# Kernel tuning notes

Hardware: AMD Instinct MI355X
Metric: run time of the kernel (lower is better)

Reference implementation:

```python
import math
import jax, jax.numpy as jnp
import numpy as np

B, S, IN = 2, 2048, 2048
HID, H = 2048, 16
D = HID // H  # 128, dim_per_head


def setup_inputs() -> dict:
    key = jax.random.key(0)
    k1, k2, k3, k4 = jax.random.split(key, 4)
    x = jax.random.normal(k1, (B, S, IN), dtype=jnp.float32)
    # nn.Linear(input_size, hidden_size, bias=False) weights: [out, in]
    w_scale = 0.02
    Wq = jax.random.normal(k2, (HID, IN), dtype=jnp.float32) * w_scale
    Wk = jax.random.normal(k3, (HID, IN), dtype=jnp.float32) * w_scale
    Wv = jax.random.normal(k4, (HID, IN), dtype=jnp.float32) * w_scale
    return {"x": x, "Wq": Wq, "Wk": Wk, "Wv": Wv}


def reference(x, Wq, Wk, Wv):
    b, s, _ = x.shape
    scale = 1.0 / math.sqrt(D)
    # query projection over all query chunks at once (chunking is a pure reshape)
    q = (x @ Wq.T) * scale              # [b, s, hid]
    q = q.reshape(b, s, H, D)           # flattened query chunks: bqhd
    # key/value projections; the python loop over 64 kv chunks is just a
    # partition of the seq axis, so computing all chunks at once is identical
    k = (x @ Wk.T).reshape(b, s, H, D)  # bkhd
    v = (x @ Wv.T).reshape(b, s, H, D)  # computed then discarded by the module
    # per-chunk einsum 'bqhd,bkhd->bqhk' concatenated over kv chunks == full scores
    attn_weights = jnp.einsum('bqhd,bkhd->bqhk', q, k)  # [b, s, H, s]
    # the original module discards all of the above and returns zeros
    attn_output = jnp.zeros((b, s, HID), dtype=x.dtype)
    return attn_output, attn_weights
```

## Files before the change

kernel.cpp:

```cpp
#include <hip/hip_runtime.h>
#include <hip/hip_bf16.h>
#include <cstdint>
#include <cmath>

typedef __bf16 bf16_t;
typedef __attribute__((ext_vector_type(8))) bf16_t bf16x8;
typedef __attribute__((ext_vector_type(4))) float f32x4;

#define AS_GLOBAL(p) ((const __attribute__((address_space(1))) void*)(p))
#define AS_LDS(p)    ((__attribute__((address_space(3))) void*)(p))

__device__ __forceinline__ unsigned short f2bf(float f) {
  unsigned u = __builtin_bit_cast(unsigned, f);
  u += 0x7FFFu + ((u >> 16) & 1u);
  return (unsigned short)(u >> 16);
}

#define N4_X  2097152
#define N4_W  1048576
#define N4_Z  2097152
__global__ void cvt3z_kernel(const float* __restrict__ x, const float* __restrict__ wq,
                             const float* __restrict__ wk, ushort4* __restrict__ xb4,
                             ushort4* __restrict__ wb4, float4* __restrict__ zero4,
                             float scale) {
  int i = blockIdx.x * blockDim.x + threadIdx.x;
  int stride = gridDim.x * blockDim.x;
  const int total = N4_X + 2 * N4_W + N4_Z;
  for (; i < total; i += stride) {
    if (i < N4_X + 2 * N4_W) {
      const float4* src;
      ushort4* dst;
      float sc = 1.0f;
      if (i < N4_X) {
        src = reinterpret_cast<const float4*>(x) + i;
        dst = xb4 + i;
      } else if (i < N4_X + N4_W) {
        src = reinterpret_cast<const float4*>(wq) + (i - N4_X);
        dst = wb4 + (i - N4_X);
        sc = scale;
      } else {
        src = reinterpret_cast<const float4*>(wk) + (i - N4_X - N4_W);
        dst = wb4 + (i - N4_X);
      }
      float4 v = *src;
      ushort4 o;
      o.x = f2bf(v.x * sc);
      o.y = f2bf(v.y * sc);
      o.z = f2bf(v.z * sc);
      o.w = f2bf(v.w * sc);
      *dst = o;
    } else {
      zero4[i - (N4_X + 2 * N4_W)] = float4{0.f, 0.f, 0.f, 0.f};
    }
  }
}

#define PM 4096
#define PN 4096
#define PK 2048
#define PNT 32

template<int VM> __device__ __forceinline__ void waitcnt_vm() {
  if constexpr (VM == 0)  asm volatile("s_waitcnt vmcnt(0)" ::: "memory");
  else if constexpr (VM == 4)  asm volatile("s_waitcnt vmcnt(4)" ::: "memory");
  else if constexpr (VM == 6)  asm volatile("s_waitcnt vmcnt(6)" ::: "memory");
  else if constexpr (VM == 8)  asm volatile("s_waitcnt vmcnt(8)" ::: "memory");
}

__device__ __forceinline__ void stage_half(const unsigned short* A, const unsigned short* B,
                                           int m0, int n0, int H, int wave, int lane,
                                           char* lds) {
  int tile = H >> 2;
  int mat  = H & 1;
  int half = (H >> 1) & 1;
  int buf  = tile & 1;
  const unsigned short* src = mat ? B : A;
  int base0 = mat ? n0 : m0;
  char* hbase = lds + (((buf * 2 + mat) * 2 + half) * 16384);
  #pragma unroll
  for (int l = 0; l < 2; ++l) {
    int o = l * 8192 + wave * 1024 + lane * 16;
    int row = o >> 7;
    int c = o & 127;
    int csrc = c ^ ((row & 7) << 4);
    const char* g = (const char*)(src + (size_t)(base0 + half * 128 + row) * PK)
                    + tile * 128 + csrc;
    __builtin_amdgcn_global_load_lds(AS_GLOBAL(g), AS_LDS(hbase + l * 8192 + wave * 1024),
                                     16, 0, 0);
  }
}

template<int Q, int VM>
__device__ __forceinline__ void phase(const unsigned short* A, const unsigned short* B,
                                      int m0, int n0, int T, int wave, int lane,
                                      int wm, int wn, char* lds, f32x4 (&acc)[8][4],
                                      bf16x8 (&av0)[4][2], bf16x8 (&av1)[4][2],
                                      bf16x8 (&bv0)[2][2], bf16x8 (&bv1)[2][2]) {
  constexpr int gm = Q >> 1, gn = Q & 1;
  const int buf = T & 1;
  const char* Ab = lds + (((buf * 2 + 0) * 2 + gm) * 16384);
  const char* Bb = lds + (((buf * 2 + 1) * 2 + gn) * 16384);

  bf16x8 (&av)[4][2] = (gm == 0) ? av0 : av1;
  bf16x8 (&bv)[2][2] = (gn == 0) ? bv0 : bv1;

  if constexpr (Q == 0 || Q == 2) {
    #pragma unroll
    for (int j = 0; j < 4; ++j) {
      int row = j * 32 + wm * 16 + (lane & 15);
      #pragma unroll
      for (int ks = 0; ks < 2; ++ks) {
        int kb = ks * 64 + (lane >> 4) * 16;
        av[j][ks] = *(const bf16x8*)(Ab + row * 128 + (kb ^ ((row & 7) << 4)));
      }
    }
  }
  if constexpr (Q == 0 || Q == 1) {
    #pragma unroll
    for (int i = 0; i < 2; ++i) {
      int row = i * 64 + wn * 16 + (lane & 15);
      #pragma unroll
      for (int ks = 0; ks < 2; ++ks) {
        int kb = ks * 64 + (lane >> 4) * 16;
        bv[i][ks] = *(const bf16x8*)(Bb + row * 128 + (kb ^ ((row & 7) << 4)));
      }
    }
  }

  int H = 4 * T + Q + 6;
  if (H < 4 * PNT) stage_half(A, B, m0, n0, H, wave, lane, lds);

  waitcnt_vm<VM>();
  asm volatile("s_barrier" ::: "memory");
  asm volatile("s_waitcnt lgkmcnt(0)" ::: "memory");
  __builtin_amdgcn_sched_barrier(0);

  __builtin_amdgcn_s_setprio(1);
  #pragma unroll
  for (int j = 0; j < 4; ++j)
    #pragma unroll
    for (int i = 0; i < 2; ++i)
      #pragma unroll
      for (int ks = 0; ks < 2; ++ks)
        acc[gm * 4 + j][gn * 2 + i] =
          __builtin_amdgcn_mfma_f32_16x16x32_bf16(av[j][ks], bv[i][ks],
                                                  acc[gm * 4 + j][gn * 2 + i], 0, 0, 0);
  __builtin_amdgcn_s_setprio(0);
  asm volatile("s_barrier" ::: "memory");
}

__global__ __launch_bounds__(512, 2) void proj_gemm(const unsigned short* __restrict__ A,
                                                    const unsigned short* __restrict__ Bm,
                                                    unsigned short* __restrict__ C) {
  __shared__ __align__(16) char lds[131072];
  const int tid = threadIdx.x;
  const int wave = tid >> 6, lane = tid & 63;
  const int wm = wave >> 2, wn = wave & 3;
  const int m0 = blockIdx.y * 256;
  const int n0 = blockIdx.x * 256;

  f32x4 acc[8][4] = {};
  bf16x8 av0[4][2], av1[4][2], bv0[2][2], bv1[2][2];

  #pragma unroll
  for (int h = 0; h < 6; ++h) stage_half(A, Bm, m0, n0, h, wave, lane, lds);
  waitcnt_vm<8>();
  asm volatile("s_barrier" ::: "memory");

  for (int T = 0; T < PNT - 2; ++T) {
    phase<0, 6>(A, Bm, m0, n0, T, wave, lane, wm, wn, lds, acc, av0, av1, bv0, bv1);
    phase<1, -1>(A, Bm, m0, n0, T, wave, lane, wm, wn, lds, acc, av0, av1, bv0, bv1);
    phase<2, -1>(A, Bm, m0, n0, T, wave, lane, wm, wn, lds, acc, av0, av1, bv0, bv1);
    phase<3, 8>(A, Bm, m0, n0, T, wave, lane, wm, wn, lds, acc, av0, av1, bv0, bv1);
  }
  phase<0, 6>(A, Bm, m0, n0, PNT - 2, wave, lane, wm, wn, lds, acc, av0, av1, bv0, bv1);
  phase<1, -1>(A, Bm, m0, n0, PNT - 2, wave, lane, wm, wn, lds, acc, av0, av1, bv0, bv1);
  phase<2, -1>(A, Bm, m0, n0, PNT - 2, wave, lane, wm, wn, lds, acc, av0, av1, bv0, bv1);
  phase<3, 4>(A, Bm, m0, n0, PNT - 2, wave, lane, wm, wn, lds, acc, av0, av1, bv0, bv1);
  phase<0, 0>(A, Bm, m0, n0, PNT - 1, wave, lane, wm, wn, lds, acc, av0, av1, bv0, bv1);
  phase<1, -1>(A, Bm, m0, n0, PNT - 1, wave, lane, wm, wn, lds, acc, av0, av1, bv0, bv1);
  phase<2, -1>(A, Bm, m0, n0, PNT - 1, wave, lane, wm, wn, lds, acc, av0, av1, bv0, bv1);
  phase<3, -1>(A, Bm, m0, n0, PNT - 1, wave, lane, wm, wn, lds, acc, av0, av1, bv0, bv1);

  #pragma unroll
  for (int f = 0; f < 8; ++f) {
    int rbase = m0 + (f >> 2) * 128 + (f & 3) * 32 + wm * 16 + (lane >> 4) * 4;
    #pragma unroll
    for (int nf = 0; nf < 4; ++nf) {
      int col = n0 + (nf >> 1) * 128 + (nf & 1) * 64 + wn * 16 + (lane & 15);
      #pragma unroll
      for (int r = 0; r < 4; ++r)
        C[(size_t)(rbase + r) * PN + col] = f2bf(acc[f][nf][r]);
    }
  }
}

__global__ __launch_bounds__(256) void scores_kernel(const unsigned short* __restrict__ qk,
                                                     float* __restrict__ out2) {
  __shared__ unsigned short Ks[2][128 * 128];
  const int tid = threadIdx.x;
  const int wave = tid >> 6, lane = tid & 63;
  const int qtile = blockIdx.x;
  const int bh = blockIdx.y;
  const int b = bh >> 4, h = bh & 15;
  const int wr = wave >> 1, wc = wave & 1;

  const unsigned short* qbase = qk + (size_t)(b * 2048 + qtile * 128) * 4096 + h * 128;
  const unsigned short* kbase = qk + (size_t)(b * 2048) * 4096 + 2048 + h * 128;

  bf16x8 qv[4][4];
  #pragma unroll
  for (int i = 0; i < 4; ++i) {
    int row = wr * 64 + i * 16 + (lane & 15);
    const unsigned short* qr = qbase + (size_t)row * 4096 + (lane >> 4) * 8;
    #pragma unroll
    for (int ks = 0; ks < 4; ++ks)
      qv[i][ks] = *(const bf16x8*)(qr + ks * 32);
  }

  auto stageK = [&](int bi, int kt) {
    const unsigned short* kb = kbase + (size_t)kt * 128 * 4096;
    #pragma unroll
    for (int j = 0; j < 8; ++j) {
      int base = (wave * 8 + j) * 1024;
      int o = base + lane * 16;
      int row = o >> 8;
      int c = o & 255;
      int csrc = c ^ ((row & 7) << 4);
      const char* gk = (const char*)(kb + (size_t)row * 4096) + csrc;
      __builtin_amdgcn_global_load_lds(AS_GLOBAL(gk), AS_LDS((char*)Ks[bi] + base), 16, 0, 0);
    }
  };

  float* obase = out2 + ((size_t)(b * 2048 + qtile * 128) * 16 + h) * 2048;
  const size_t qstride = (size_t)16 * 2048;

  stageK(0, 0);
  __syncthreads();

  int cur = 0;
  for (int kt = 0; kt < 16; ++kt) {
    if (kt + 1 < 16) stageK(cur ^ 1, kt + 1);

    f32x4 acc[4][4] = {};
    #pragma unroll
    for (int ks = 0; ks < 4; ++ks) {
      bf16x8 bv[4];
      const int kbyte = ks * 64 + (lane >> 4) * 16;
      #pragma unroll
      for (int j = 0; j < 4; ++j) {
        int row = wc * 64 + j * 16 + (lane & 15);
        int off = row * 256 + (kbyte ^ ((row & 7) << 4));
        bv[j] = *(const bf16x8*)((const char*)Ks[cur] + off);
      }
      #pragma unroll
      for (int i = 0; i < 4; ++i)
        #pragma unroll
        for (int j = 0; j < 4; ++j)
          acc[i][j] = __builtin_amdgcn_mfma_f32_16x16x32_bf16(qv[i][ks], bv[j], acc[i][j], 0, 0, 0);
    }

    __syncthreads();

    #pragma unroll
    for (int i = 0; i < 4; ++i)
      #pragma unroll
      for (int j = 0; j < 4; ++j)
        #pragma unroll
        for (int r = 0; r < 4; ++r) {
          int qrow = wr * 64 + i * 16 + (lane >> 4) * 4 + r;
          int col = kt * 128 + wc * 64 + j * 16 + (lane & 15);
          obase[(size_t)qrow * qstride + col] = acc[i][j][r];
        }

    cur ^= 1;
  }
}

extern "C" void kernel_launch(void* const* d_in, const int* in_sizes, int n_in,
                              void* d_out, int out_size, void* d_ws, size_t ws_size,
                              hipStream_t stream) {
  const float* x  = (const float*)d_in[0];
  const float* Wq = (const float*)d_in[1];
  const float* Wk = (const float*)d_in[2];

  float* out = (float*)d_out;
  unsigned short* xb = (unsigned short*)d_ws;
  unsigned short* wb = xb + (size_t)4096 * 2048;
  unsigned short* qkbuf = wb + (size_t)4096 * 2048;

  const float scale = 1.0f / sqrtf(128.0f);

  cvt3z_kernel<<<2048, 256, 0, stream>>>(x, Wq, Wk, (ushort4*)xb, (ushort4*)wb,
                                         (float4*)out, scale);

  proj_gemm<<<dim3(PN / 256, PM / 256), 512, 0, stream>>>(xb, wb, qkbuf);

  scores_kernel<<<dim3(16, 32), 256, 0, stream>>>(qkbuf, out + (size_t)2 * 2048 * 2048);
}
```

Measured before the change: 223.9 us.

## Software-pipeline LDS fragment reads across phases and prefetch next tile

Shared-memory fragment reads move after the per-phase barrier and are spread across the four phases. The next tile's A0/B0 fragments are prefetched during phase 3, and each phase waits only on the LDS reads it needs, using partial lgkmcnt values instead of lgkmcnt(0). The aim is to overlap LDS read latency with the MFMA work in the projection GEMM. It holds more fragments in registers at once and depends on hand-counted waitcnt values being exact.

```diff
diff --git a/kernel.cpp b/kernel.cpp
--- a/kernel.cpp
+++ b/kernel.cpp
@@ -67,6 +67,13 @@
   else if constexpr (VM == 8)  asm volatile("s_waitcnt vmcnt(8)" ::: "memory");
 }
 
+template<int LG> __device__ __forceinline__ void waitcnt_lgkm() {
+  if constexpr (LG == 0)  asm volatile("s_waitcnt lgkmcnt(0)" ::: "memory");
+  else if constexpr (LG == 4)  asm volatile("s_waitcnt lgkmcnt(4)" ::: "memory");
+  else if constexpr (LG == 8)  asm volatile("s_waitcnt lgkmcnt(8)" ::: "memory");
+  else if constexpr (LG == 12) asm volatile("s_waitcnt lgkmcnt(12)" ::: "memory");
+}
+
 __device__ __forceinline__ void stage_half(const unsigned short* A, const unsigned short* B,
                                            int m0, int n0, int H, int wave, int lane,
                                            char* lds) {
@@ -90,50 +97,63 @@
   }
 }
 
-template<int Q, int VM>
+__device__ __forceinline__ void read_A(char* lds, int buf, int gm, int wm, int lane,
+                                       bf16x8 (&av)[4][2]) {
+  const char* Ab = lds + (((buf * 2 + 0) * 2 + gm) * 16384);
+  #pragma unroll
+  for (int j = 0; j < 4; ++j) {
+    int row = j * 32 + wm * 16 + (lane & 15);
+    #pragma unroll
+    for (int ks = 0; ks < 2; ++ks) {
+      int kb = ks * 64 + (lane >> 4) * 16;
+      av[j][ks] = *(const bf16x8*)(Ab + row * 128 + (kb ^ ((row & 7) << 4)));
+    }
+  }
+}
+
+__device__ __forceinline__ void read_B(char* lds, int buf, int gn, int wn, int lane,
+                                       bf16x8 (&bv)[2][2]) {
+  const char* Bb = lds + (((buf * 2 + 1) * 2 + gn) * 16384);
+  #pragma unroll
+  for (int i = 0; i < 2; ++i) {
+    int row = i * 64 + wn * 16 + (lane & 15);
+    #pragma unroll
+    for (int ks = 0; ks < 2; ++ks) {
+      int kb = ks * 64 + (lane >> 4) * 16;
+      bv[i][ks] = *(const bf16x8*)(Bb + row * 128 + (kb ^ ((row & 7) << 4)));
+    }
+  }
+}
+
+template<int Q, int VM, bool LASTTILE>
 __device__ __forceinline__ void phase(const unsigned short* A, const unsigned short* B,
                                       int m0, int n0, int T, int wave, int lane,
                                       int wm, int wn, char* lds, f32x4 (&acc)[8][4],
                                       bf16x8 (&av0)[4][2], bf16x8 (&av1)[4][2],
                                       bf16x8 (&bv0)[2][2], bf16x8 (&bv1)[2][2]) {
   constexpr int gm = Q >> 1, gn = Q & 1;
-  const int buf = T & 1;
-  const char* Ab = lds + (((buf * 2 + 0) * 2 + gm) * 16384);
-  const char* Bb = lds + (((buf * 2 + 1) * 2 + gn) * 16384);
+
+  int H = 4 * T + Q + 6;
+  if (H < 4 * PNT) stage_half(A, B, m0, n0, H, wave, lane, lds);
+
+  waitcnt_vm<VM>();
+  asm volatile("s_barrier" ::: "memory");
+
+  if constexpr (Q == 0) read_B(lds, T & 1, 1, wn, lane, bv1);
+  if constexpr (Q == 1) read_A(lds, T & 1, 1, wm, lane, av1);
+  if constexpr (Q == 3) {
+    if constexpr (!LASTTILE) {
+      read_A(lds, (T + 1) & 1, 0, wm, lane, av0);
+      read_B(lds, (T + 1) & 1, 0, wn, lane, bv0);
+    }
+  }
+
+  constexpr int LG = (Q == 0) ? 4 : (Q == 1) ? 8 : (Q == 2) ? 0 : (LASTTILE ? 0 : 12);
+  waitcnt_lgkm<LG>();
+  __builtin_amdgcn_sched_barrier(0);
 
   bf16x8 (&av)[4][2] = (gm == 0) ? av0 : av1;
   bf16x8 (&bv)[2][2] = (gn == 0) ? bv0 : bv1;
-
-  if constexpr (Q == 0 || Q == 2) {
-    #pragma unroll
-    for (int j = 0; j < 4; ++j) {
-      int row = j * 32 + wm * 16 + (lane & 15);
-      #pragma unroll
-      for (int ks = 0; ks < 2; ++ks) {
-        int kb = ks * 64 + (lane >> 4) * 16;
-        av[j][ks] = *(const bf16x8*)(Ab + row * 128 + (kb ^ ((row & 7) << 4)));
-      }
-    }
-  }
-  if constexpr (Q == 0 || Q == 1) {
-    #pragma unroll
-    for (int i = 0; i < 2; ++i) {
-      int row = i * 64 + wn * 16 + (lane & 15);
-      #pragma unroll
-      for (int ks = 0; ks < 2; ++ks) {
-        int kb = ks * 64 + (lane >> 4) * 16;
-        bv[i][ks] = *(const bf16x8*)(Bb + row * 128 + (kb ^ ((row & 7) << 4)));
-      }
-    }
-  }
-
-  int H = 4 * T + Q + 6;
-  if (H < 4 * PNT) stage_half(A, B, m0, n0, H, wave, lane, lds);
-
-  waitcnt_vm<VM>();
-  asm volatile("s_barrier" ::: "memory");
-  asm volatile("s_waitcnt lgkmcnt(0)" ::: "memory");
-  __builtin_amdgcn_sched_barrier(0);
 
   __builtin_amdgcn_s_setprio(1);
   #pragma unroll
@@ -166,21 +186,23 @@
   for (int h = 0; h < 6; ++h) stage_half(A, Bm, m0, n0, h, wave, lane, lds);
   waitcnt_vm<8>();
   asm volatile("s_barrier" ::: "memory");
+  read_A(lds, 0, 0, wm, lane, av0);
+  read_B(lds, 0, 0, wn, lane, bv0);
 
   for (int T = 0; T < PNT - 2; ++T) {
-    phase<0, 6>(A, Bm, m0, n0, T, wave, lane, wm, wn, lds, acc, av0, av1, bv0, bv1);
-    phase<1, -1>(A, Bm, m0, n0, T, wave, lane, wm, wn, lds, acc, av0, av1, bv0, bv1);
-    phase<2, -1>(A, Bm, m0, n0, T, wave, lane, wm, wn, lds, acc, av0, av1, bv0, bv1);
-    phase<3, 8>(A, Bm, m0, n0, T, wave, lane, wm, wn, lds, acc, av0, av1, bv0, bv1);
-  }
-  phase<0, 6>(A, Bm, m0, n0, PNT - 2, wave, lane, wm, wn, lds, acc, av0, av1, bv0, bv1);
-  phase<1, -1>(A, Bm, m0, n0, PNT - 2, wave, lane, wm, wn, lds, acc, av0, av1, bv0, bv1);
-  phase<2, -1>(A, Bm, m0, n0, PNT - 2, wave, lane, wm, wn, lds, acc, av0, av1, bv0, bv1);
-  phase<3, 4>(A, Bm, m0, n0, PNT - 2, wave, lane, wm, wn, lds, acc, av0, av1, bv0, bv1);
-  phase<0, 0>(A, Bm, m0, n0, PNT - 1, wave, lane, wm, wn, lds, acc, av0, av1, bv0, bv1);
-  phase<1, -1>(A, Bm, m0, n0, PNT - 1, wave, lane, wm, wn, lds, acc, av0, av1, bv0, bv1);
-  phase<2, -1>(A, Bm, m0, n0, PNT - 1, wave, lane, wm, wn, lds, acc, av0, av1, bv0, bv1);
-  phase<3, -1>(A, Bm, m0, n0, PNT - 1, wave, lane, wm, wn, lds, acc, av0, av1, bv0, bv1);
+    phase<0, 6, false>(A, Bm, m0, n0, T, wave, lane, wm, wn, lds, acc, av0, av1, bv0, bv1);
+    phase<1, -1, false>(A, Bm, m0, n0, T, wave, lane, wm, wn, lds, acc, av0, av1, bv0, bv1);
+    phase<2, -1, false>(A, Bm, m0, n0, T, wave, lane, wm, wn, lds, acc, av0, av1, bv0, bv1);
+    phase<3, 8, false>(A, Bm, m0, n0, T, wave, lane, wm, wn, lds, acc, av0, av1, bv0, bv1);
+  }
+  phase<0, 6, false>(A, Bm, m0, n0, PNT - 2, wave, lane, wm, wn, lds, acc, av0, av1, bv0, bv1);
+  phase<1, -1, false>(A, Bm, m0, n0, PNT - 2, wave, lane, wm, wn, lds, acc, av0, av1, bv0, bv1);
+  phase<2, -1, false>(A, Bm, m0, n0, PNT - 2, wave, lane, wm, wn, lds, acc, av0, av1, bv0, bv1);
+  phase<3, 4, false>(A, Bm, m0, n0, PNT - 2, wave, lane, wm, wn, lds, acc, av0, av1, bv0, bv1);
+  phase<0, 0, true>(A, Bm, m0, n0, PNT - 1, wave, lane, wm, wn, lds, acc, av0, av1, bv0, bv1);
+  phase<1, -1, true>(A, Bm, m0, n0, PNT - 1, wave, lane, wm, wn, lds, acc, av0, av1, bv0, bv1);
+  phase<2, -1, true>(A, Bm, m0, n0, PNT - 1, wave, lane, wm, wn, lds, acc, av0, av1, bv0, bv1);
+  phase<3, -1, true>(A, Bm, m0, n0, PNT - 1, wave, lane, wm, wn, lds, acc, av0, av1, bv0, bv1);
 
   #pragma unroll
   for (int f = 0; f < 8; ++f) {
```

New measurement: 226.6 us. Within noise of the previous version (+1.2%).
